# Kernel optimization log

Hardware: AMD Instinct MI355X
Metric: run time of the kernel (lower is better)

Reference implementation:

```python
import jax, jax.numpy as jnp
import numpy as np

NUM_TOKENS = 8192
EMBED_DIM = 32
BETA = 1.0
DECAY = 0.99
L2_EPS = 1e-12  # torch F.normalize denom clamp


def l2norm(t):
    return t / jnp.maximum(jnp.linalg.norm(t, axis=-1, keepdims=True), L2_EPS)


def setup_inputs() -> dict:
    key = jax.random.key(0)
    k1, k2 = jax.random.split(key)
    z = jax.random.normal(k1, (32, EMBED_DIM, 16, 16), dtype=jnp.float32)  # [B, C, H, W]
    embedding = l2norm(jax.random.normal(k2, (NUM_TOKENS, EMBED_DIM), dtype=jnp.float32))
    cluster_sizes = jnp.zeros((NUM_TOKENS,), dtype=jnp.float32)
    return {"z": z, "embedding": embedding, "cluster_sizes": cluster_sizes}


def reference(z, embedding, cluster_sizes):
    B, C, H, W = z.shape
    zc = jnp.transpose(z, (0, 2, 3, 1))          # channel_last: [B, H, W, C]
    zn = l2norm(zc)
    z_flat = zn.reshape(-1, C)                   # [N, C], N = B*H*W

    # nearest centroid by cosine similarity (codebook rows are unit norm)
    cos_sim = z_flat @ embedding.T               # [N, K]
    token_ids = jnp.argmax(cos_sim, axis=-1)     # [N]
    z_q_flat = embedding[token_ids]              # gather, [N, C]
    z_q = z_q_flat.reshape(zn.shape)

    # EMA statistics (training branch; one-hot @ matmuls expressed as scatter-adds)
    bins = jnp.zeros((NUM_TOKENS,), z.dtype).at[token_ids].add(1.0)      # encodings.sum(0)
    new_cluster_sizes = cluster_sizes * DECAY + (1.0 - DECAY) * bins
    zero_mask = bins == 0
    bins_c = jnp.where(zero_mask, 1.0, bins)
    embed_sum = jnp.zeros((NUM_TOKENS, C), z.dtype).at[token_ids].add(z_flat)  # (z_flat.T @ onehot).T
    embed_normalized = l2norm(embed_sum / bins_c[:, None])
    embed_normalized = jnp.where(zero_mask[:, None], embedding, embed_normalized)
    new_embedding = l2norm(embedding * DECAY + (1.0 - DECAY) * embed_normalized)

    # commitment loss + straight-through estimator
    loss = BETA * jnp.mean((jax.lax.stop_gradient(z_q) - zn) ** 2)
    z_q_st = zn + jax.lax.stop_gradient(z_q - zn)
    z_q_out = jnp.transpose(z_q_st, (0, 3, 1, 2))  # back to [B, C, H, W]

    return (z_q_out, loss, token_ids.reshape(B, H, W), new_embedding, new_cluster_sizes)
```

## Files before the change

### kernel.cpp

```cpp
#include <hip/hip_runtime.h>


#define NTOK   8192
#define NCODE  8192
#define CDIM   32
#define HW     256
#define DECAYF 0.99f
#define EPSF   0.01f

#define OUT_ZQ   0
#define OUT_LOSS 262144
#define OUT_IDS  262145
#define OUT_EMB  270337
#define OUT_CS   532481

#define WS_ZN     0u
#define WS_ZNBF   1048576u
#define WS_EBF    1572864u
#define WS_PMAX   2097152u
#define WS_PACK   3145728u
#define WS_EMBT   3211264u

#define CHUNK  256
#define NCHUNK (NCODE / CHUNK)
#define TILES  (CHUNK / 16)

typedef __attribute__((ext_vector_type(8))) short bf16x8;
typedef __attribute__((ext_vector_type(4))) float f32x4;

__device__ inline unsigned short f2bf(float x) {
    unsigned u = __float_as_uint(x);
    return (unsigned short)((u + 0x7FFFu + ((u >> 16) & 1u)) >> 16);
}
__device__ inline unsigned fmap(float s) {
    unsigned u = __float_as_uint(s);
    return (u & 0x80000000u) ? ~u : (u | 0x80000000u);
}

__device__ inline void stage_chunk(const unsigned short* __restrict__ ebf,
                                   int kbase, float4* lbs5, int t) {
    const float4* src = (const float4*)(ebf + (size_t)kbase * CDIM);
#pragma unroll
    for (int j = 0; j < 4; ++j) {
        int u = t + j * 256;
        int row = u >> 2, seg = u & 3;
        lbs5[row * 5 + seg] = src[u];
    }
}

__global__ __launch_bounds__(256) void k_prep(const float* __restrict__ z,
                                              const float* __restrict__ emb,
                                              float* __restrict__ zn,
                                              unsigned short* __restrict__ znbf,
                                              unsigned short* __restrict__ ebf,
                                              float* __restrict__ embT,
                                              float* __restrict__ out) {
    __shared__ float tile[32][65];
    int bid = blockIdx.x, t = threadIdx.x;
    if (bid < 32) {
        int n = bid * 256 + t;
        int b = n >> 8, hw = n & 255;
        const float* zp = z + (size_t)b * (CDIM * HW) + hw;
        float v[CDIM];
        float ss = 0.f;
#pragma unroll
        for (int c = 0; c < CDIM; ++c) {
            float tv = zp[c * HW];
            v[c] = tv;
            ss += tv * tv;
        }
        float d = fmaxf(sqrtf(ss), 1e-12f);
        float* o = zn + (size_t)n * CDIM;
        unsigned short* ob = znbf + (size_t)n * CDIM;
#pragma unroll
        for (int c = 0; c < CDIM; ++c) {
            float tv = v[c] / d;
            o[c] = tv;
            ob[c] = f2bf(tv);
        }
    } else if (bid < 160) {
        int blk = bid - 32;
        int r0 = blk * 64;
        int base = blk * 2048 + t * 8;
        const float4* s = (const float4*)(emb + base);
        float4 x4 = s[0], y4 = s[1];
        ushort4 u0 = {f2bf(x4.x), f2bf(x4.y), f2bf(x4.z), f2bf(x4.w)};
        ushort4 u1 = {f2bf(y4.x), f2bf(y4.y), f2bf(y4.z), f2bf(y4.w)};
        *(ushort4*)(ebf + base) = u0;
        *(ushort4*)(ebf + base + 4) = u1;
        int lr = t >> 2, c0 = (t & 3) * 8;
        tile[c0 + 0][lr] = x4.x; tile[c0 + 1][lr] = x4.y;
        tile[c0 + 2][lr] = x4.z; tile[c0 + 3][lr] = x4.w;
        tile[c0 + 4][lr] = y4.x; tile[c0 + 5][lr] = y4.y;
        tile[c0 + 6][lr] = y4.z; tile[c0 + 7][lr] = y4.w;
        __syncthreads();
        int c = t >> 3, seg = t & 7;
        float4 w0 = {tile[c][seg * 8 + 0], tile[c][seg * 8 + 1],
                     tile[c][seg * 8 + 2], tile[c][seg * 8 + 3]};
        float4 w1 = {tile[c][seg * 8 + 4], tile[c][seg * 8 + 5],
                     tile[c][seg * 8 + 6], tile[c][seg * 8 + 7]};
        float* dst = embT + (size_t)c * NCODE + r0 + seg * 8;
        *(float4*)dst = w0;
        *(float4*)(dst + 4) = w1;
    } else {
        if (t == 0) out[OUT_LOSS] = 0.f;
    }
}

__global__ __launch_bounds__(256) void k_max(const unsigned short* __restrict__ znbf,
                                             const unsigned short* __restrict__ ebf,
                                             float* __restrict__ pmaxT) {
    __shared__ float4 lbs5[CHUNK * 5];
    __shared__ float lmax[256];
    int kbase = blockIdx.y * CHUNK;
    stage_chunk(ebf, kbase, lbs5, threadIdx.x);
    __syncthreads();

    int wave = threadIdx.x >> 6, lane = threadIdx.x & 63;
    int col = lane & 15, quad = lane >> 4;
    int wtok = blockIdx.x * 256 + wave * 64;

    bf16x8 a[4];
#pragma unroll
    for (int f = 0; f < 4; ++f)
        a[f] = *(const bf16x8*)(znbf + (size_t)(wtok + f * 16 + col) * CDIM + quad * 8);

    const bf16x8* bl = (const bf16x8*)lbs5;
    const f32x4 zero4 = {0.f, 0.f, 0.f, 0.f};
    float m[4][4];
#pragma unroll
    for (int f = 0; f < 4; ++f)
#pragma unroll
        for (int r = 0; r < 4; ++r) m[f][r] = -1e30f;

    for (int t = 0; t < TILES; ++t) {
        bf16x8 b = bl[(t * 16 + col) * 5 + quad];
#pragma unroll
        for (int f = 0; f < 4; ++f) {
            f32x4 d = __builtin_amdgcn_mfma_f32_16x16x32_bf16(a[f], b, zero4, 0, 0, 0);
#pragma unroll
            for (int r = 0; r < 4; ++r) m[f][r] = fmaxf(m[f][r], d[r]);
        }
    }
#pragma unroll
    for (int f = 0; f < 4; ++f)
#pragma unroll
        for (int r = 0; r < 4; ++r) {
            float v = m[f][r];
#pragma unroll
            for (int s = 1; s < 16; s <<= 1) v = fmaxf(v, __shfl_xor(v, s));
            if (col == 0) lmax[wave * 64 + f * 16 + quad * 4 + r] = v;
        }
    __syncthreads();
    pmaxT[(size_t)(blockIdx.x * 256 + threadIdx.x) * NCHUNK + blockIdx.y] =
        lmax[threadIdx.x];
}

__global__ __launch_bounds__(256) void k_rescan(const float* __restrict__ zn,
                                                const float* __restrict__ embT,
                                                const float* __restrict__ pmaxT,
                                                unsigned long long* __restrict__ packed) {
    int wave = threadIdx.x >> 6, lane = threadIdx.x & 63;
    int n = blockIdx.x * 4 + wave;

    float pm = -1e30f;
    if (lane < 32) pm = pmaxT[(size_t)n * NCHUNK + lane];
    float mx = pm;
#pragma unroll
    for (int s = 1; s < 64; s <<= 1) mx = fmaxf(mx, __shfl_xor(mx, s));
    float thr = mx - EPSF;
    unsigned m32 = (unsigned)(__ballot(pm >= thr) & 0xFFFFFFFFull);

    float zr[CDIM];
    const float4* zp4 = (const float4*)(zn + (size_t)n * CDIM);
#pragma unroll
    for (int j = 0; j < 8; ++j) {
        float4 v4 = zp4[j];
        zr[4 * j + 0] = v4.x;
        zr[4 * j + 1] = v4.y;
        zr[4 * j + 2] = v4.z;
        zr[4 * j + 3] = v4.w;
    }

    unsigned long long kbest = 0ull;
    while (m32) {
        int ch = __ffs(m32) - 1;
        m32 &= m32 - 1;
        const float* bp = embT + ch * CHUNK + 4 * lane;
        float acc[4][4] = {};
#pragma unroll
        for (int c = 0; c < CDIM; ++c) {
            float4 e4 = *(const float4*)(bp + (size_t)c * NCODE);
            int r = c & 3;
            acc[r][0] = __builtin_fmaf(zr[c], e4.x, acc[r][0]);
            acc[r][1] = __builtin_fmaf(zr[c], e4.y, acc[r][1]);
            acc[r][2] = __builtin_fmaf(zr[c], e4.z, acc[r][2]);
            acc[r][3] = __builtin_fmaf(zr[c], e4.w, acc[r][3]);
        }
#pragma unroll
        for (int j = 0; j < 4; ++j) {
            float s = (acc[0][j] + acc[1][j]) + (acc[2][j] + acc[3][j]);
            int code = ch * CHUNK + 4 * lane + j;
            unsigned long long key = ((unsigned long long)fmap(s) << 13) |
                                     (unsigned long long)(8191 - code);
            kbest = kbest > key ? kbest : key;
        }
    }
#pragma unroll
    for (int s = 1; s < 64; s <<= 1) {
        unsigned long long o = __shfl_xor(kbest, s);
        kbest = kbest > o ? kbest : o;
    }
    if (lane == 0) packed[n] = kbest;
}

__global__ __launch_bounds__(256) void k_final(const unsigned long long* __restrict__ packed,
                                               const float* __restrict__ zn,
                                               const float* __restrict__ emb,
                                               const float* __restrict__ cs,
                                               float* __restrict__ out) {
    __shared__ float lesum[32][32];
    __shared__ int lbins[32];
    __shared__ int lsid[32];
    __shared__ float ls4[4];

    int blk = blockIdx.x, t = threadIdx.x;
    int wave = t >> 6, lane = t & 63;
    int tok0 = blk * 32, kbase = blk * 32;

    if (t < 32) lbins[t] = 0;
#pragma unroll
    for (int i = 0; i < 4; ++i) {
        int idx = i * 256 + t;
        lesum[idx >> 5][idx & 31] = 0.f;
    }
    if (t < 32) {
        int n = tok0 + t;
        int id = 8191 - (int)(packed[n] & 8191ull);
        lsid[t] = id;
        out[OUT_IDS + n] = (float)id;
    }
    __syncthreads();

    float s = 0.f;
#pragma unroll
    for (int i = 0; i < 4; ++i) {
        int idx = i * 256 + t;
        int tl = idx >> 5, c = idx & 31;
        int n = tok0 + tl;
        int id = lsid[tl];
        float ev = emb[(size_t)id * CDIM + c];
        float zv = zn[(size_t)n * CDIM + c];
        int b = n >> 8, hw = n & 255;
        out[OUT_ZQ + ((size_t)b * CDIM + c) * HW + hw] = ev;
        float dd = ev - zv;
        s += dd * dd;
    }
#pragma unroll
    for (int off = 32; off > 0; off >>= 1) s += __shfl_down(s, off);
    if (lane == 0) ls4[wave] = s;
    __syncthreads();
    if (t == 0)
        atomicAdd(out + OUT_LOSS,
                  (ls4[0] + ls4[1] + ls4[2] + ls4[3]) * (1.0f / 262144.0f));

    for (int i = 0; i < 32; ++i) {
        int n = i * 256 + t;
        int id = 8191 - (int)(packed[n] & 8191ull);
        unsigned kl = (unsigned)(id - kbase);
        if (kl < 32u) {
            atomicAdd(&lbins[kl], 1);
            const float* zp = zn + (size_t)n * CDIM;
#pragma unroll
            for (int c = 0; c < CDIM; ++c)
                atomicAdd(&lesum[kl][c], zp[c]);
        }
    }
    __syncthreads();

#pragma unroll
    for (int i = 0; i < 4; ++i) {
        int idx = i * 256 + t;
        int kl = idx >> 5, c = idx & 31;
        int k = kbase + kl;
        int bi = lbins[kl];
        float bf = (float)bi;
        bool zero = (bi == 0);
        float tv = lesum[kl][c] / (zero ? 1.0f : bf);
        float ss = tv * tv;
#pragma unroll
        for (int sh = 1; sh < 32; sh <<= 1) ss += __shfl_xor(ss, sh);
        float d = fmaxf(sqrtf(ss), 1e-12f);
        float ew = emb[(size_t)k * CDIM + c];
        float en = zero ? ew : (tv / d);
        float w = ew * DECAYF + (1.0f - DECAYF) * en;
        float ss2 = w * w;
#pragma unroll
        for (int sh = 1; sh < 32; sh <<= 1) ss2 += __shfl_xor(ss2, sh);
        float d2 = fmaxf(sqrtf(ss2), 1e-12f);
        out[OUT_EMB + (size_t)k * CDIM + c] = w / d2;
        if (c == 0) out[OUT_CS + k] = cs[k] * DECAYF + (1.0f - DECAYF) * bf;
    }
}

extern "C" void kernel_launch(void* const* d_in, const int* in_sizes, int n_in,
                              void* d_out, int out_size, void* d_ws, size_t ws_size,
                              hipStream_t stream) {
    const float* z   = (const float*)d_in[0];
    const float* emb = (const float*)d_in[1];
    const float* cs  = (const float*)d_in[2];
    float* out = (float*)d_out;
    char* ws = (char*)d_ws;

    float* zn                  = (float*)(ws + WS_ZN);
    unsigned short* znbf       = (unsigned short*)(ws + WS_ZNBF);
    unsigned short* ebf        = (unsigned short*)(ws + WS_EBF);
    float* pmaxT               = (float*)(ws + WS_PMAX);
    unsigned long long* packed = (unsigned long long*)(ws + WS_PACK);
    float* embT                = (float*)(ws + WS_EMBT);

    k_prep<<<dim3(161), 256, 0, stream>>>(z, emb, zn, znbf, ebf, embT, out);
    k_max<<<dim3(NTOK / 256, NCHUNK), 256, 0, stream>>>(znbf, ebf, pmaxT);
    k_rescan<<<dim3(NTOK / 4), 256, 0, stream>>>(zn, embT, pmaxT, packed);
    k_final<<<dim3(256), 256, 0, stream>>>(packed, zn, emb, cs, out);
}
```

Measured before the change: 143.0 us.

## Fuse VQ pipeline into a single cooperative kernel with grid syncs

Replaces the four-kernel sequence (prep, chunked bf16 max, fp32 rescan, final EMA) with one cooperative kernel of 512 blocks that uses grid.sync between phases. Each block converts its pair of codebook chunks to bf16 in LDS once and reuses them for both the max pass and the rescan. The rescan recomputes the MFMA scores and runs an exact fp32 dot product only for candidates above the threshold, merging winners with a 64-bit atomicMax. This targets kernel launch gaps and the separate full-precision rescan, at the cost of three grid-wide barriers and a final phase where every block scans all token ids. It falls back to the old kernels if cooperative launch is unavailable.

After: 143.0 us. No clear change (+0.0%).

```diff
diff --git a/kernel.cpp b/kernel.cpp
--- a/kernel.cpp
+++ b/kernel.cpp
@@ -1,4 +1,7 @@
 #include <hip/hip_runtime.h>
+#include <hip/hip_cooperative_groups.h>
+
+namespace cg = cooperative_groups;
 
 
 #define NTOK   8192
@@ -37,6 +40,243 @@
     return (u & 0x80000000u) ? ~u : (u | 0x80000000u);
 }
 
+__global__ __launch_bounds__(256) void k_fused(
+    const float* __restrict__ z, const float* __restrict__ emb,
+    const float* __restrict__ cs, float* __restrict__ zn,
+    unsigned short* __restrict__ znbf, float* __restrict__ pmax,
+    unsigned long long* __restrict__ packed, float* __restrict__ out) {
+    __shared__ float4 lbs5[2 * CHUNK * 5];
+    __shared__ float lmax[256];
+    __shared__ float lesum[16][32];
+    __shared__ int lbins[16];
+    __shared__ int lsid[16];
+    __shared__ float ls4[4];
+
+    cg::grid_group grid = cg::this_grid();
+    const int t = threadIdx.x, bid = blockIdx.x;
+    const int bx = bid & 31;
+    const int cpair = bid >> 5;
+    const int kb0 = cpair * (2 * CHUNK);
+
+#pragma unroll
+    for (int cc = 0; cc < 2; ++cc) {
+        const float* src = emb + (size_t)(kb0 + cc * CHUNK) * CDIM;
+        float4* dst = lbs5 + cc * CHUNK * 5;
+#pragma unroll
+        for (int j = 0; j < 4; ++j) {
+            int u = t + j * 256, row = u >> 2, seg = u & 3;
+            const float4* p = (const float4*)(src + row * CDIM + seg * 8);
+            float4 x4 = p[0], y4 = p[1];
+            union { float4 f4; unsigned short us[8]; } w;
+            w.us[0] = f2bf(x4.x); w.us[1] = f2bf(x4.y);
+            w.us[2] = f2bf(x4.z); w.us[3] = f2bf(x4.w);
+            w.us[4] = f2bf(y4.x); w.us[5] = f2bf(y4.y);
+            w.us[6] = f2bf(y4.z); w.us[7] = f2bf(y4.w);
+            dst[row * 5 + seg] = w.f4;
+        }
+    }
+
+    if (bid < 32) {
+        int n = bid * 256 + t;
+        int b = n >> 8, hw = n & 255;
+        const float* zp = z + (size_t)b * (CDIM * HW) + hw;
+        float v[CDIM];
+        float ss = 0.f;
+#pragma unroll
+        for (int c = 0; c < CDIM; ++c) {
+            float tv = zp[c * HW];
+            v[c] = tv;
+            ss += tv * tv;
+        }
+        float dn = fmaxf(sqrtf(ss), 1e-12f);
+        float* o = zn + (size_t)n * CDIM;
+        unsigned short* ob = znbf + (size_t)n * CDIM;
+#pragma unroll
+        for (int c = 0; c < CDIM; ++c) {
+            float tv = v[c] / dn;
+            o[c] = tv;
+            ob[c] = f2bf(tv);
+        }
+    } else if (bid < 36) {
+        int base = (bid - 32) * 2048 + t;
+#pragma unroll
+        for (int j = 0; j < 8; ++j) packed[base + j * 256] = 0ull;
+    } else if (bid == 36) {
+        if (t == 0) out[OUT_LOSS] = 0.f;
+    }
+
+    __syncthreads();
+    grid.sync();
+
+    const int wave = t >> 6, lane = t & 63;
+    const int col = lane & 15, quad = lane >> 4;
+    const int wtok = bx * 256 + wave * 64;
+
+    bf16x8 a[4];
+#pragma unroll
+    for (int f = 0; f < 4; ++f)
+        a[f] = *(const bf16x8*)(znbf + (size_t)(wtok + f * 16 + col) * CDIM + quad * 8);
+
+    const f32x4 zero4 = {0.f, 0.f, 0.f, 0.f};
+#pragma unroll 1
+    for (int cc = 0; cc < 2; ++cc) {
+        const bf16x8* bl = (const bf16x8*)(lbs5 + cc * CHUNK * 5);
+        float m[4][4];
+#pragma unroll
+        for (int f = 0; f < 4; ++f)
+#pragma unroll
+            for (int r = 0; r < 4; ++r) m[f][r] = -1e30f;
+        for (int tt = 0; tt < TILES; ++tt) {
+            bf16x8 b = bl[(tt * 16 + col) * 5 + quad];
+#pragma unroll
+            for (int f = 0; f < 4; ++f) {
+                f32x4 d = __builtin_amdgcn_mfma_f32_16x16x32_bf16(a[f], b, zero4, 0, 0, 0);
+#pragma unroll
+                for (int r = 0; r < 4; ++r) m[f][r] = fmaxf(m[f][r], d[r]);
+            }
+        }
+#pragma unroll
+        for (int f = 0; f < 4; ++f)
+#pragma unroll
+            for (int r = 0; r < 4; ++r) {
+                float v = m[f][r];
+#pragma unroll
+                for (int s = 1; s < 16; s <<= 1) v = fmaxf(v, __shfl_xor(v, s));
+                if (col == 0) lmax[wave * 64 + f * 16 + quad * 4 + r] = v;
+            }
+        __syncthreads();
+        pmax[(size_t)(cpair * 2 + cc) * NTOK + bx * 256 + t] = lmax[t];
+        __syncthreads();
+    }
+    grid.sync();
+
+    {
+        int tok = bx * 256 + t;
+        float mx = -1e30f;
+#pragma unroll
+        for (int ch = 0; ch < NCHUNK; ++ch)
+            mx = fmaxf(mx, pmax[(size_t)ch * NTOK + tok]);
+        lmax[t] = mx - EPSF;
+    }
+    __syncthreads();
+
+    float thr[4][4];
+#pragma unroll
+    for (int f = 0; f < 4; ++f)
+#pragma unroll
+        for (int r = 0; r < 4; ++r)
+            thr[f][r] = lmax[wave * 64 + f * 16 + quad * 4 + r];
+
+#pragma unroll 1
+    for (int cc = 0; cc < 2; ++cc) {
+        const bf16x8* bl = (const bf16x8*)(lbs5 + cc * CHUNK * 5);
+        const int kbase = kb0 + cc * CHUNK;
+        for (int tt = 0; tt < TILES; ++tt) {
+            bf16x8 b = bl[(tt * 16 + col) * 5 + quad];
+#pragma unroll
+            for (int f = 0; f < 4; ++f) {
+                f32x4 d = __builtin_amdgcn_mfma_f32_16x16x32_bf16(a[f], b, zero4, 0, 0, 0);
+#pragma unroll
+                for (int r = 0; r < 4; ++r) {
+                    if (d[r] >= thr[f][r]) {
+                        int tok = wtok + f * 16 + quad * 4 + r;
+                        int code = kbase + tt * 16 + col;
+                        const float* zp = zn + (size_t)tok * CDIM;
+                        const float* ep = emb + (size_t)code * CDIM;
+                        float a0 = 0.f, a1 = 0.f, a2 = 0.f, a3 = 0.f;
+#pragma unroll
+                        for (int j = 0; j < 8; ++j) {
+                            a0 = __builtin_fmaf(zp[4 * j + 0], ep[4 * j + 0], a0);
+                            a1 = __builtin_fmaf(zp[4 * j + 1], ep[4 * j + 1], a1);
+                            a2 = __builtin_fmaf(zp[4 * j + 2], ep[4 * j + 2], a2);
+                            a3 = __builtin_fmaf(zp[4 * j + 3], ep[4 * j + 3], a3);
+                        }
+                        float sc = (a0 + a1) + (a2 + a3);
+                        atomicMax(packed + tok,
+                                  ((unsigned long long)fmap(sc) << 13) |
+                                  (unsigned long long)(8191 - code));
+                    }
+                }
+            }
+        }
+    }
+    grid.sync();
+
+    if (t < 16) lbins[t] = 0;
+#pragma unroll
+    for (int i = 0; i < 2; ++i) {
+        int idx = i * 256 + t;
+        lesum[idx >> 5][idx & 31] = 0.f;
+    }
+    const int tok0 = bid * 16, kb2 = bid * 16;
+    if (t < 16) {
+        int n = tok0 + t;
+        int id = 8191 - (int)(packed[n] & 8191ull);
+        lsid[t] = id;
+        out[OUT_IDS + n] = (float)id;
+    }
+    __syncthreads();
+
+    float s = 0.f;
+#pragma unroll
+    for (int i = 0; i < 2; ++i) {
+        int idx = i * 256 + t;
+        int tl = idx >> 5, c = idx & 31;
+        int n = tok0 + tl;
+        int id = lsid[tl];
+        float ev = emb[(size_t)id * CDIM + c];
+        float zv = zn[(size_t)n * CDIM + c];
+        int b = n >> 8, hw = n & 255;
+        out[OUT_ZQ + ((size_t)b * CDIM + c) * HW + hw] = ev;
+        float dd = ev - zv;
+        s += dd * dd;
+    }
+#pragma unroll
+    for (int off = 32; off > 0; off >>= 1) s += __shfl_down(s, off);
+    if (lane == 0) ls4[wave] = s;
+
+    for (int i = 0; i < 32; ++i) {
+        int n = i * 256 + t;
+        int id = 8191 - (int)(packed[n] & 8191ull);
+        unsigned kl = (unsigned)(id - kb2);
+        if (kl < 16u) {
+            atomicAdd(&lbins[kl], 1);
+            const float* zp = zn + (size_t)n * CDIM;
+#pragma unroll
+            for (int c = 0; c < CDIM; ++c)
+                atomicAdd(&lesum[kl][c], zp[c]);
+        }
+    }
+    __syncthreads();
+    if (t == 0)
+        atomicAdd(out + OUT_LOSS,
+                  (ls4[0] + ls4[1] + ls4[2] + ls4[3]) * (1.0f / 262144.0f));
+
+#pragma unroll
+    for (int i = 0; i < 2; ++i) {
+        int idx = i * 256 + t;
+        int kl = idx >> 5, c = idx & 31;
+        int k = kb2 + kl;
+        int bi = lbins[kl];
+        float bf = (float)bi;
+        bool zero = (bi == 0);
+        float tv = lesum[kl][c] / (zero ? 1.0f : bf);
+        float ss = tv * tv;
+#pragma unroll
+        for (int sh = 1; sh < 32; sh <<= 1) ss += __shfl_xor(ss, sh);
+        float dn = fmaxf(sqrtf(ss), 1e-12f);
+        float ew = emb[(size_t)k * CDIM + c];
+        float en = zero ? ew : (tv / dn);
+        float w = ew * DECAYF + (1.0f - DECAYF) * en;
+        float ss2 = w * w;
+#pragma unroll
+        for (int sh = 1; sh < 32; sh <<= 1) ss2 += __shfl_xor(ss2, sh);
+        float d2 = fmaxf(sqrtf(ss2), 1e-12f);
+        out[OUT_EMB + (size_t)k * CDIM + c] = w / d2;
+        if (c == 0) out[OUT_CS + k] = cs[k] * DECAYF + (1.0f - DECAYF) * bf;
+    }
+}
+
 __device__ inline void stage_chunk(const unsigned short* __restrict__ ebf,
                                    int kbase, float4* lbs5, int t) {
     const float4* src = (const float4*)(ebf + (size_t)kbase * CDIM);
@@ -48,7 +288,7 @@
     }
 }
 
-__global__ __launch_bounds__(256) void k_prep(const float* __restrict__ z,
+__global__ __launch_bounds__(256) void p_prep(const float* __restrict__ z,
                                               const float* __restrict__ emb,
                                               float* __restrict__ zn,
                                               unsigned short* __restrict__ znbf,
@@ -107,7 +347,7 @@
     }
 }
 
-__global__ __launch_bounds__(256) void k_max(const unsigned short* __restrict__ znbf,
+__global__ __launch_bounds__(256) void p_max(const unsigned short* __restrict__ znbf,
                                              const unsigned short* __restrict__ ebf,
                                              float* __restrict__ pmaxT) {
     __shared__ float4 lbs5[CHUNK * 5];
@@ -156,7 +396,7 @@
         lmax[threadIdx.x];
 }
 
-__global__ __launch_bounds__(256) void k_rescan(const float* __restrict__ zn,
+__global__ __launch_bounds__(256) void p_rescan(const float* __restrict__ zn,
                                                 const float* __restrict__ embT,
                                                 const float* __restrict__ pmaxT,
                                                 unsigned long long* __restrict__ packed) {
@@ -214,7 +454,7 @@
     if (lane == 0) packed[n] = kbest;
 }
 
-__global__ __launch_bounds__(256) void k_final(const unsigned long long* __restrict__ packed,
+__global__ __launch_bounds__(256) void p_final(const unsigned long long* __restrict__ packed,
                                                const float* __restrict__ zn,
                                                const float* __restrict__ emb,
                                                const float* __restrict__ cs,
@@ -315,12 +555,30 @@
     float* zn                  = (float*)(ws + WS_ZN);
     unsigned short* znbf       = (unsigned short*)(ws + WS_ZNBF);
     unsigned short* ebf        = (unsigned short*)(ws + WS_EBF);
-    float* pmaxT               = (float*)(ws + WS_PMAX);
+    float* pmax                = (float*)(ws + WS_PMAX);
     unsigned long long* packed = (unsigned long long*)(ws + WS_PACK);
     float* embT                = (float*)(ws + WS_EMBT);
 
-    k_prep<<<dim3(161), 256, 0, stream>>>(z, emb, zn, znbf, ebf, embT, out);
-    k_max<<<dim3(NTOK / 256, NCHUNK), 256, 0, stream>>>(znbf, ebf, pmaxT);
-    k_rescan<<<dim3(NTOK / 4), 256, 0, stream>>>(zn, embT, pmaxT, packed);
-    k_final<<<dim3(256), 256, 0, stream>>>(packed, zn, emb, cs, out);
-}
+    static int coop = -1;
+    if (coop < 0) {
+        int nb = 0;
+        hipError_t e = hipOccupancyMaxActiveBlocksPerMultiprocessor(&nb, k_fused, 256, 0);
+        coop = (e == hipSuccess && nb >= 2) ? 1 : 0;
+        if (e != hipSuccess) (void)hipGetLastError();
+    }
+
+    if (coop) {
+        void* args[] = {(void*)&z, (void*)&emb, (void*)&cs, (void*)&zn,
+                        (void*)&znbf, (void*)&pmax, (void*)&packed, (void*)&out};
+        hipError_t e = hipLaunchCooperativeKernel(k_fused, dim3(512), dim3(256),
+                                                  args, 0, stream);
+        if (e == hipSuccess) return;
+        (void)hipGetLastError();
+        coop = 0;
+    }
+
+    p_prep<<<dim3(161), 256, 0, stream>>>(z, emb, zn, znbf, ebf, embT, out);
+    p_max<<<dim3(NTOK / 256, NCHUNK), 256, 0, stream>>>(znbf, ebf, pmax);
+    p_rescan<<<dim3(NTOK / 4), 256, 0, stream>>>(zn, embT, pmax, packed);
+    p_final<<<dim3(256), 256, 0, stream>>>(packed, zn, emb, cs, out);
+}
```
